# Optimization experiments

Hardware: AMD Instinct MI355X
Metric: run time of the kernel (lower is better)

The kernel has to match this reference:

```python
import jax, jax.numpy as jnp
import numpy as np
from jax import lax

INPUT_DIM = 16
H1, H2 = 64, 32
OUT_DIM = 1
B, T = 4096, 168


def _uniform(key, shape, k):
    return jax.random.uniform(key, shape, jnp.float32, -k, k)


def setup_inputs() -> dict:
    key = jax.random.key(0)
    ks = jax.random.split(key, 12)
    k1 = 1.0 / np.sqrt(H1)
    k2 = 1.0 / np.sqrt(H2)
    return {
        "x": jax.random.normal(ks[0], (B, T, INPUT_DIM), jnp.float32),
        # layer 1 (PyTorch gate order: i, f, g, o)
        "W_ih1": _uniform(ks[1], (4 * H1, INPUT_DIM), k1),
        "W_hh1": _uniform(ks[2], (4 * H1, H1), k1),
        "b_ih1": _uniform(ks[3], (4 * H1,), k1),
        "b_hh1": _uniform(ks[4], (4 * H1,), k1),
        # layer 2
        "W_ih2": _uniform(ks[5], (4 * H2, H1), k2),
        "W_hh2": _uniform(ks[6], (4 * H2, H2), k2),
        "b_ih2": _uniform(ks[7], (4 * H2,), k2),
        "b_hh2": _uniform(ks[8], (4 * H2,), k2),
        # final linear
        "W_fc": _uniform(ks[9], (OUT_DIM, H2), k2),
        "b_fc": _uniform(ks[10], (OUT_DIM,), k2),
    }


def _lstm(x, W_ih, W_hh, b_ih, b_hh, hidden):
    # Precompute input-to-gate projections for all timesteps: [B, T, 4H]
    xg = jnp.einsum("btd,gd->btg", x, W_ih) + b_ih + b_hh

    def step(carry, xt):
        h, c = carry
        gates = xt + h @ W_hh.T  # [B, 4H]
        i, f, g, o = jnp.split(gates, 4, axis=-1)
        i = jax.nn.sigmoid(i)
        f = jax.nn.sigmoid(f)
        g = jnp.tanh(g)
        o = jax.nn.sigmoid(o)
        c = f * c + i * g
        h = o * jnp.tanh(c)
        return (h, c), h

    bsz = x.shape[0]
    init = (jnp.zeros((bsz, hidden), x.dtype), jnp.zeros((bsz, hidden), x.dtype))
    (_, _), hs = lax.scan(step, init, jnp.swapaxes(xg, 0, 1))  # hs: [T, B, H]
    return jnp.swapaxes(hs, 0, 1)  # [B, T, H]


def reference(x, W_ih1, W_hh1, b_ih1, b_hh1, W_ih2, W_hh2, b_ih2, b_hh2, W_fc, b_fc):
    # Dropout layers are identity at inference (p=0.2 in train only).
    h1 = _lstm(x, W_ih1, W_hh1, b_ih1, b_hh1, H1)   # [B, T, 64]
    h2 = _lstm(h1, W_ih2, W_hh2, b_ih2, b_hh2, H2)  # [B, T, 32]
    last = h2[:, -1, :]                              # [B, 32]
    return last @ W_fc.T + b_fc                      # [B, OUT_DIM]
```

## Files before the change

kernel.cpp:

```cpp
#include <hip/hip_runtime.h>


typedef __bf16 bf16x8 __attribute__((ext_vector_type(8)));
typedef float  f32x4  __attribute__((ext_vector_type(4)));

constexpr int T_SEQ = 168;
constexpr int NB    = 16;

__device__ __forceinline__ float fsig(float v)  { return __builtin_amdgcn_rcpf(1.f + __expf(-v)); }
__device__ __forceinline__ float ftanhf(float v){ return 2.f * __builtin_amdgcn_rcpf(1.f + __expf(-2.f * v)) - 1.f; }

__device__ __forceinline__ void split_bf16(float x, __bf16& hi, __bf16& lo) {
  hi = (__bf16)x;
  lo = (__bf16)(x - (float)hi);
}

__device__ __forceinline__ void load_frag8(const float* __restrict__ Wrow, int k0,
                                           bf16x8& hi, bf16x8& lo) {
#pragma unroll
  for (int j = 0; j < 8; ++j) {
    float v = Wrow[k0 + j];
    __bf16 h = (__bf16)v;
    hi[j] = h;
    lo[j] = (__bf16)(v - (float)h);
  }
}

#define MFMA(a, b, c) __builtin_amdgcn_mfma_f32_16x16x32_bf16((a), (b), (c), 0, 0, 0)

__global__ __launch_bounds__(512) __attribute__((amdgpu_waves_per_eu(2, 2)))
void lstm_mfma_kernel(const float* __restrict__ x,
    const float* __restrict__ Wih1, const float* __restrict__ Whh1,
    const float* __restrict__ bih1, const float* __restrict__ bhh1,
    const float* __restrict__ Wih2, const float* __restrict__ Whh2,
    const float* __restrict__ bih2, const float* __restrict__ bhh2,
    const float* __restrict__ Wfc,  const float* __restrict__ bfc,
    float* __restrict__ out)
{
  __shared__ __align__(16) __bf16 sA1[2][4 * 64 * 8];
  __shared__ __align__(16) __bf16 sA2[2][2 * 64 * 8];
  __shared__ __align__(16) __bf16 sW2lo[8 * 2 * 64 * 8];
  __shared__ __align__(16) float  sP[2][2 * 4 * 64 * 4];
  __shared__ __align__(16) float  sH2f[16 * 32];

  const int tid  = threadIdx.x;
  const int w    = tid >> 6;
  const int lane = tid & 63;
  const int q    = lane >> 4;
  const int col  = lane & 15;
  const int b0   = blockIdx.x * NB;

  const bool isL1  = (w < 4);
  const bool isL2b = (w == 4) || (w == 5);
  const bool isL2a = (w >= 6);
  const int  wl2b  = w - 4;
  const int  wl2a  = w - 6;

  bf16x8 bhh[4][4];
  bf16x8 bih[4];
  float  b1v[4] = {0.f, 0.f, 0.f, 0.f};
  if (isL1) {
#pragma unroll
    for (int g = 0; g < 4; ++g) {
      const int r = g * 64 + w * 16 + col;
      const float* Wr = Whh1 + r * 64;
      bf16x8 h0, l0, h1f, l1f;
      load_frag8(Wr, 0 * 32 + q * 8, h0, l0);
      load_frag8(Wr, 1 * 32 + q * 8, h1f, l1f);
      bhh[g][0] = h0; bhh[g][1] = h1f; bhh[g][2] = l0; bhh[g][3] = l1f;
      bf16x8 xh, xl;
      load_frag8(Wih1 + r * 16, (q & 1) * 8, xh, xl);
      bih[g] = (q < 2) ? xh : xl;
      b1v[g] = bih1[r] + bhh1[r];
    }
  }
  bf16x8 wh2h[4], wh2l[4];
  float  b2v[4] = {0.f, 0.f, 0.f, 0.f};
  if (isL2b) {
#pragma unroll
    for (int g = 0; g < 4; ++g) {
      const int r = g * 32 + wl2b * 16 + col;
      bf16x8 hh, ll;
      load_frag8(Whh2 + r * 32, q * 8, hh, ll);
      wh2h[g] = hh; wh2l[g] = ll;
      b2v[g] = bih2[r] + bhh2[r];
    }
  }
  bf16x8 w2ih[4][2];
  if (isL2a) {
#pragma unroll
    for (int g = 0; g < 4; ++g) {
      const int r = g * 32 + wl2a * 16 + col;
#pragma unroll
      for (int kb = 0; kb < 2; ++kb) {
        bf16x8 hh, ll;
        load_frag8(Wih2 + r * 64, kb * 32 + q * 8, hh, ll);
        w2ih[g][kb] = hh;
      }
    }
  }

  for (int idx = tid; idx < 8 * 2 * 64; idx += 512) {
    const int nt  = idx >> 7;
    const int kb2 = (idx >> 6) & 1;
    const int ln  = idx & 63;
    const int qq  = ln >> 4, cc = ln & 15;
    const int g   = nt >> 1, wv = nt & 1;
    const int r   = g * 32 + wv * 16 + cc;
    const int k0  = kb2 * 32 + qq * 8;
    bf16x8 hh, ll;
    load_frag8(Wih2 + r * 64, k0, hh, ll);
    *(bf16x8*)&sW2lo[((nt * 2 + kb2) * 64 + ln) * 8] = ll;
  }

  {
    bf16x8 z;
#pragma unroll
    for (int j = 0; j < 8; ++j) z[j] = (__bf16)0.f;
    for (int i = tid; i < 2 * 4 * 64; i += 512) *(bf16x8*)&sA1[0][i * 8] = z;
    for (int i = tid; i < 2 * 2 * 64; i += 512) *(bf16x8*)&sA2[0][i * 8] = z;
  }
  __syncthreads();

  const float* xbase = x + ((size_t)(b0 + col) * T_SEQ) * 16 + (q & 1) * 8;
  float4 xcA, xcB, xnA, xnB;
  if (isL1) {
    xcA = *(const float4*)(xbase + 0);
    xcB = *(const float4*)(xbase + 4);
  }

  float c1s[4] = {0.f, 0.f, 0.f, 0.f};
  float c2s[4] = {0.f, 0.f, 0.f, 0.f};
  const int uu   = w * 16 + col;
  const int uu2b = wl2b * 16 + col;

  const int kbh  = uu >> 5;
  const int lnb  = ((uu & 31) >> 3) * 16;
  const int jj   = uu & 7;
  const int lnb2 = ((uu2b & 31) >> 3) * 16;
  const int jj2  = uu2b & 7;

#define STEP(Pc, DO_L1, DO_XPRE, DO_L2A, DO_L2B, DO_H2F, TT) do {              \
    if ((DO_L1) && isL1) {                                                     \
      bf16x8 a1[4];                                                            \
      _Pragma("unroll")                                                        \
      for (int kb = 0; kb < 4; ++kb)                                           \
        a1[kb] = *(const bf16x8*)&sA1[(Pc)][(kb * 64 + lane) * 8];             \
      if (DO_XPRE) {                                                           \
        const float* xr = xbase + (size_t)((TT) + 1) * 16;                     \
        xnA = *(const float4*)(xr + 0);                                        \
        xnB = *(const float4*)(xr + 4);                                        \
      }                                                                        \
      const float xc[8] = {xcA.x, xcA.y, xcA.z, xcA.w, xcB.x, xcB.y, xcB.z, xcB.w}; \
      bf16x8 xh8, xl8;                                                         \
      _Pragma("unroll")                                                        \
      for (int j = 0; j < 8; ++j) {                                            \
        __bf16 h_, l_; split_bf16(xc[j], h_, l_);                              \
        xh8[j] = h_; xl8[j] = l_;                                              \
      }                                                                        \
      const bf16x8 ax0 = (q < 2) ? xh8 : xl8;                                  \
      const bf16x8 ax1 = (q < 2) ? xl8 : xh8;                                  \
      f32x4 ca[4], cb[4];                                                      \
      _Pragma("unroll")                                                        \
      for (int g = 0; g < 4; ++g) {                                            \
        ca[g][0] = b1v[g]; ca[g][1] = b1v[g]; ca[g][2] = b1v[g]; ca[g][3] = b1v[g]; \
        cb[g][0] = 0.f; cb[g][1] = 0.f; cb[g][2] = 0.f; cb[g][3] = 0.f;        \
      }                                                                        \
      _Pragma("unroll")                                                        \
      for (int g = 0; g < 4; ++g) {                                            \
        ca[g] = MFMA(ax0,   bih[g],    ca[g]);                                 \
        ca[g] = MFMA(ax1,   bih[g],    ca[g]);                                 \
        ca[g] = MFMA(a1[0], bhh[g][0], ca[g]);                                 \
        ca[g] = MFMA(a1[1], bhh[g][1], ca[g]);                                 \
        cb[g] = MFMA(a1[2], bhh[g][0], cb[g]);                                 \
        cb[g] = MFMA(a1[3], bhh[g][1], cb[g]);                                 \
        cb[g] = MFMA(a1[0], bhh[g][2], cb[g]);                                 \
        cb[g] = MFMA(a1[1], bhh[g][3], cb[g]);                                 \
      }                                                                        \
      _Pragma("unroll")                                                        \
      for (int r = 0; r < 4; ++r) {                                            \
        const float iv = fsig(ca[0][r] + cb[0][r]);                            \
        const float fv = fsig(ca[1][r] + cb[1][r]);                            \
        const float gv = ftanhf(ca[2][r] + cb[2][r]);                          \
        const float ov = fsig(ca[3][r] + cb[3][r]);                            \
        const float cc = fmaf(fv, c1s[r], iv * gv);                            \
        c1s[r] = cc;                                                           \
        __bf16 hh_, hl_;                                                       \
        split_bf16(ov * ftanhf(cc), hh_, hl_);                                 \
        const int m = q * 4 + r;                                               \
        sA1[1 - (Pc)][((kbh * 64) + lnb + m) * 8 + jj]       = hh_;            \
        sA1[1 - (Pc)][(((2 + kbh) * 64) + lnb + m) * 8 + jj] = hl_;            \
      }                                                                        \
      if (DO_XPRE) { xcA = xnA; xcB = xnB; }                                   \
    }                                                                          \
    if ((DO_L2A) && isL2a) {                                                   \
      bf16x8 a2[4];                                                            \
      _Pragma("unroll")                                                        \
      for (int kb = 0; kb < 4; ++kb)                                           \
        a2[kb] = *(const bf16x8*)&sA1[(Pc)][(kb * 64 + lane) * 8];             \
      _Pragma("unroll")                                                        \
      for (int g = 0; g < 4; ++g) {                                            \
        const int nt = g * 2 + wl2a;                                           \
        const bf16x8 bb2 = *(const bf16x8*)&sW2lo[((nt * 2 + 0) * 64 + lane) * 8]; \
        const bf16x8 bb3 = *(const bf16x8*)&sW2lo[((nt * 2 + 1) * 64 + lane) * 8]; \
        f32x4 pa = {0.f, 0.f, 0.f, 0.f};                                       \
        pa = MFMA(a2[0], w2ih[g][0], pa);                         \
        pa = MFMA(a2[1], w2ih[g][1], pa);                                      \
        pa = MFMA(a2[0], bb2, pa);                                \
        pa = MFMA(a2[1], bb3, pa);                                             \
        pa = MFMA(a2[2], w2ih[g][0], pa);                         \
        pa = MFMA(a2[3], w2ih[g][1], pa);                                      \
        *(f32x4*)&sP[(Pc)][((wl2a * 4 + g) * 64 + lane) * 4] = pa;             \
      }                                                                        \
    }                                                                          \
    if ((DO_L2B) && isL2b) {                                                   \
      const bf16x8 ah0 = *(const bf16x8*)&sA2[1 - (Pc)][(0 * 64 + lane) * 8];  \
      const bf16x8 ah1 = *(const bf16x8*)&sA2[1 - (Pc)][(1 * 64 + lane) * 8];  \
      f32x4 c2[4];                                                             \
      _Pragma("unroll")                                                        \
      for (int g = 0; g < 4; ++g) {                                            \
        c2[g][0] = b2v[g]; c2[g][1] = b2v[g]; c2[g][2] = b2v[g]; c2[g][3] = b2v[g]; \
        c2[g] = MFMA(ah0, wh2h[g], c2[g]);                                     \
        c2[g] = MFMA(ah1, wh2h[g], c2[g]);                                     \
        c2[g] = MFMA(ah0, wh2l[g], c2[g]);                                     \
        c2[g] += *(const f32x4*)&sP[1 - (Pc)][((wl2b * 4 + g) * 64 + lane) * 4]; \
      }                                                                        \
      _Pragma("unroll")                                                        \
      for (int r = 0; r < 4; ++r) {                                            \
        const float iv = fsig(c2[0][r]);                                       \
        const float fv = fsig(c2[1][r]);                                       \
        const float gv = ftanhf(c2[2][r]);                                     \
        const float ov = fsig(c2[3][r]);                                       \
        const float cc = fmaf(fv, c2s[r], iv * gv);                            \
        c2s[r] = cc;                                                           \
        const float hf = ov * ftanhf(cc);                                      \
        __bf16 hh_, hl_;                                                       \
        split_bf16(hf, hh_, hl_);                                              \
        const int m = q * 4 + r;                                               \
        sA2[(Pc)][((0 * 64) + lnb2 + m) * 8 + jj2] = hh_;                      \
        sA2[(Pc)][((1 * 64) + lnb2 + m) * 8 + jj2] = hl_;                      \
        if (DO_H2F) sH2f[m * 32 + uu2b] = hf;                                  \
      }                                                                        \
    }                                                                          \
    __syncthreads();                                                           \
  } while (0)

  STEP(0, true,  true,  false, false, false, 0);
  STEP(1, true,  true,  true,  false, false, 1);
  for (int t = 2; t < 166; t += 2) {
    STEP(0, true, true, true, true, false, t);
    STEP(1, true, true, true, true, false, t + 1);
  }
  STEP(0, true,  true,  true,  true,  false, 166);
  STEP(1, true,  false, true,  true,  false, 167);
  STEP(0, false, false, true,  true,  false, 168);
  STEP(1, false, false, false, true,  true,  169);
#undef STEP

  if (tid < NB) {
    float s = bfc[0];
#pragma unroll
    for (int j = 0; j < 32; ++j) s = fmaf(Wfc[j], sH2f[tid * 32 + j], s);
    out[b0 + tid] = s;
  }
}

extern "C" void kernel_launch(void* const* d_in, const int* in_sizes, int n_in,
                              void* d_out, int out_size, void* d_ws, size_t ws_size,
                              hipStream_t stream) {
  (void)in_sizes; (void)n_in; (void)out_size; (void)d_ws; (void)ws_size;
  const float* x    = (const float*)d_in[0];
  const float* Wih1 = (const float*)d_in[1];
  const float* Whh1 = (const float*)d_in[2];
  const float* bih1 = (const float*)d_in[3];
  const float* bhh1 = (const float*)d_in[4];
  const float* Wih2 = (const float*)d_in[5];
  const float* Whh2 = (const float*)d_in[6];
  const float* bih2 = (const float*)d_in[7];
  const float* bhh2 = (const float*)d_in[8];
  const float* Wfc  = (const float*)d_in[9];
  const float* bfc  = (const float*)d_in[10];
  float* out = (float*)d_out;

  hipLaunchKernelGGL(lstm_mfma_kernel, dim3(4096 / NB), dim3(512), 0, stream,
                     x, Wih1, Whh1, bih1, bhh1, Wih2, Whh2, bih2, bhh2, Wfc, bfc, out);
}
```

Measured before the change: 273.5 us.

## Offload layer-1 input projection to layer-2 waves via shared-memory staging

Moves the per-step x·W_ih1 + bias projection off the layer-1 waves, which sit on the critical recurrent path, onto the four layer-2 waves. Those waves compute the projection one step ahead and store it in a double-buffered shared array (sXG). Layer-1 waves then load it as the MFMA accumulator seed, which removes two MFMAs per gate plus the x split work from their step. The cost is extra LDS traffic and more MFMA and global-load work on the layer-2 waves, which could lengthen their part of each step.

Result: slower. 288.1 us (+5.3%).

```diff
diff --git a/kernel.cpp b/kernel.cpp
--- a/kernel.cpp
+++ b/kernel.cpp
@@ -41,6 +41,7 @@
   __shared__ __align__(16) __bf16 sA2[2][2 * 64 * 8];
   __shared__ __align__(16) __bf16 sW2lo[8 * 2 * 64 * 8];
   __shared__ __align__(16) float  sP[2][2 * 4 * 64 * 4];
+  __shared__ __align__(16) float  sXG[2][16 * 64 * 4];
   __shared__ __align__(16) float  sH2f[16 * 32];
 
   const int tid  = threadIdx.x;
@@ -51,14 +52,14 @@
   const int b0   = blockIdx.x * NB;
 
   const bool isL1  = (w < 4);
+  const bool isL2  = (w >= 4);
   const bool isL2b = (w == 4) || (w == 5);
   const bool isL2a = (w >= 6);
   const int  wl2b  = w - 4;
   const int  wl2a  = w - 6;
+  const int  tbase = (w - 4) * 4;
 
   bf16x8 bhh[4][4];
-  bf16x8 bih[4];
-  float  b1v[4] = {0.f, 0.f, 0.f, 0.f};
   if (isL1) {
 #pragma unroll
     for (int g = 0; g < 4; ++g) {
@@ -68,10 +69,6 @@
       load_frag8(Wr, 0 * 32 + q * 8, h0, l0);
       load_frag8(Wr, 1 * 32 + q * 8, h1f, l1f);
       bhh[g][0] = h0; bhh[g][1] = h1f; bhh[g][2] = l0; bhh[g][3] = l1f;
-      bf16x8 xh, xl;
-      load_frag8(Wih1 + r * 16, (q & 1) * 8, xh, xl);
-      bih[g] = (q < 2) ? xh : xl;
-      b1v[g] = bih1[r] + bhh1[r];
     }
   }
   bf16x8 wh2h[4], wh2l[4];
@@ -97,6 +94,18 @@
         load_frag8(Wih2 + r * 64, kb * 32 + q * 8, hh, ll);
         w2ih[g][kb] = hh;
       }
+    }
+  }
+  bf16x8 wxg[4];
+  float  bxg[4] = {0.f, 0.f, 0.f, 0.f};
+  if (isL2) {
+#pragma unroll
+    for (int i = 0; i < 4; ++i) {
+      const int row = (tbase + i) * 16 + col;
+      bf16x8 hh, ll;
+      load_frag8(Wih1 + row * 16, (q & 1) * 8, hh, ll);
+      wxg[i] = (q < 2) ? hh : ll;
+      bxg[i] = bih1[row] + bhh1[row];
     }
   }
 
@@ -120,14 +129,33 @@
     for (int i = tid; i < 2 * 4 * 64; i += 512) *(bf16x8*)&sA1[0][i * 8] = z;
     for (int i = tid; i < 2 * 2 * 64; i += 512) *(bf16x8*)&sA2[0][i * 8] = z;
   }
-  __syncthreads();
 
   const float* xbase = x + ((size_t)(b0 + col) * T_SEQ) * 16 + (q & 1) * 8;
   float4 xcA, xcB, xnA, xnB;
-  if (isL1) {
+  if (isL2) {
     xcA = *(const float4*)(xbase + 0);
     xcB = *(const float4*)(xbase + 4);
-  }
+    const float xcv[8] = {xcA.x, xcA.y, xcA.z, xcA.w, xcB.x, xcB.y, xcB.z, xcB.w};
+    bf16x8 xh8, xl8;
+#pragma unroll
+    for (int j = 0; j < 8; ++j) {
+      __bf16 h_, l_; split_bf16(xcv[j], h_, l_);
+      xh8[j] = h_; xl8[j] = l_;
+    }
+    const bf16x8 ax0 = (q < 2) ? xh8 : xl8;
+    const bf16x8 ax1 = (q < 2) ? xl8 : xh8;
+#pragma unroll
+    for (int i = 0; i < 4; ++i) {
+      f32x4 cx;
+      cx[0] = bxg[i]; cx[1] = bxg[i]; cx[2] = bxg[i]; cx[3] = bxg[i];
+      cx = MFMA(ax0, wxg[i], cx);
+      cx = MFMA(ax1, wxg[i], cx);
+      *(f32x4*)&sXG[0][(((tbase + i) * 64) + lane) * 4] = cx;
+    }
+    xcA = *(const float4*)(xbase + 16);
+    xcB = *(const float4*)(xbase + 20);
+  }
+  __syncthreads();
 
   float c1s[4] = {0.f, 0.f, 0.f, 0.f};
   float c2s[4] = {0.f, 0.f, 0.f, 0.f};
@@ -140,42 +168,27 @@
   const int lnb2 = ((uu2b & 31) >> 3) * 16;
   const int jj2  = uu2b & 7;
 
-#define STEP(Pc, DO_L1, DO_XPRE, DO_L2A, DO_L2B, DO_H2F, TT) do {              \
+  const f32x4 z4 = {0.f, 0.f, 0.f, 0.f};
+
+#define STEP(Pc, DO_L1, DO_XPRE, DO_XG, DO_L2A, DO_L2B, DO_H2F, TT) do {       \
     if ((DO_L1) && isL1) {                                                     \
       bf16x8 a1[4];                                                            \
       _Pragma("unroll")                                                        \
       for (int kb = 0; kb < 4; ++kb)                                           \
         a1[kb] = *(const bf16x8*)&sA1[(Pc)][(kb * 64 + lane) * 8];             \
-      if (DO_XPRE) {                                                           \
-        const float* xr = xbase + (size_t)((TT) + 1) * 16;                     \
-        xnA = *(const float4*)(xr + 0);                                        \
-        xnB = *(const float4*)(xr + 4);                                        \
-      }                                                                        \
-      const float xc[8] = {xcA.x, xcA.y, xcA.z, xcA.w, xcB.x, xcB.y, xcB.z, xcB.w}; \
-      bf16x8 xh8, xl8;                                                         \
-      _Pragma("unroll")                                                        \
-      for (int j = 0; j < 8; ++j) {                                            \
-        __bf16 h_, l_; split_bf16(xc[j], h_, l_);                              \
-        xh8[j] = h_; xl8[j] = l_;                                              \
-      }                                                                        \
-      const bf16x8 ax0 = (q < 2) ? xh8 : xl8;                                  \
-      const bf16x8 ax1 = (q < 2) ? xl8 : xh8;                                  \
+      f32x4 xg[4];                                                             \
+      _Pragma("unroll")                                                        \
+      for (int g = 0; g < 4; ++g)                                              \
+        xg[g] = *(const f32x4*)&sXG[(Pc)][(((g * 4 + w) * 64) + lane) * 4];    \
       f32x4 ca[4], cb[4];                                                      \
       _Pragma("unroll")                                                        \
       for (int g = 0; g < 4; ++g) {                                            \
-        ca[g][0] = b1v[g]; ca[g][1] = b1v[g]; ca[g][2] = b1v[g]; ca[g][3] = b1v[g]; \
-        cb[g][0] = 0.f; cb[g][1] = 0.f; cb[g][2] = 0.f; cb[g][3] = 0.f;        \
-      }                                                                        \
-      _Pragma("unroll")                                                        \
-      for (int g = 0; g < 4; ++g) {                                            \
-        ca[g] = MFMA(ax0,   bih[g],    ca[g]);                                 \
-        ca[g] = MFMA(ax1,   bih[g],    ca[g]);                                 \
-        ca[g] = MFMA(a1[0], bhh[g][0], ca[g]);                                 \
-        ca[g] = MFMA(a1[1], bhh[g][1], ca[g]);                                 \
-        cb[g] = MFMA(a1[2], bhh[g][0], cb[g]);                                 \
-        cb[g] = MFMA(a1[3], bhh[g][1], cb[g]);                                 \
-        cb[g] = MFMA(a1[0], bhh[g][2], cb[g]);                                 \
-        cb[g] = MFMA(a1[1], bhh[g][3], cb[g]);                                 \
+        ca[g] = MFMA(a1[0], bhh[g][0], xg[g]);                \
+        ca[g] = MFMA(a1[1], bhh[g][1], ca[g]);                \
+        ca[g] = MFMA(a1[2], bhh[g][0], ca[g]);                \
+        cb[g] = MFMA(a1[3], bhh[g][1], z4);                   \
+        cb[g] = MFMA(a1[0], bhh[g][2], cb[g]);                \
+        cb[g] = MFMA(a1[1], bhh[g][3], cb[g]);                \
       }                                                                        \
       _Pragma("unroll")                                                        \
       for (int r = 0; r < 4; ++r) {                                            \
@@ -191,7 +204,6 @@
         sA1[1 - (Pc)][((kbh * 64) + lnb + m) * 8 + jj]       = hh_;            \
         sA1[1 - (Pc)][(((2 + kbh) * 64) + lnb + m) * 8 + jj] = hl_;            \
       }                                                                        \
-      if (DO_XPRE) { xcA = xnA; xcB = xnB; }                                   \
     }                                                                          \
     if ((DO_L2A) && isL2a) {                                                   \
       bf16x8 a2[4];                                                            \
@@ -242,19 +254,44 @@
         if (DO_H2F) sH2f[m * 32 + uu2b] = hf;                                  \
       }                                                                        \
     }                                                                          \
+    if ((DO_XG) && isL2) {                \
+      if (DO_XPRE) {                                                           \
+        const float* xr = xbase + (size_t)((TT) + 2) * 16;                     \
+        xnA = *(const float4*)(xr + 0);                                        \
+        xnB = *(const float4*)(xr + 4);                                        \
+      }                                                                        \
+      const float xcv[8] = {xcA.x, xcA.y, xcA.z, xcA.w, xcB.x, xcB.y, xcB.z, xcB.w}; \
+      bf16x8 xh8, xl8;                                                         \
+      _Pragma("unroll")                                                        \
+      for (int j = 0; j < 8; ++j) {                                            \
+        __bf16 h_, l_; split_bf16(xcv[j], h_, l_);                             \
+        xh8[j] = h_; xl8[j] = l_;                                              \
+      }                                                                        \
+      const bf16x8 ax0 = (q < 2) ? xh8 : xl8;                                  \
+      const bf16x8 ax1 = (q < 2) ? xl8 : xh8;                                  \
+      _Pragma("unroll")                                                        \
+      for (int i = 0; i < 4; ++i) {                                            \
+        f32x4 cx;                                                              \
+        cx[0] = bxg[i]; cx[1] = bxg[i]; cx[2] = bxg[i]; cx[3] = bxg[i];        \
+        cx = MFMA(ax0, wxg[i], cx);                                            \
+        cx = MFMA(ax1, wxg[i], cx);                                            \
+        *(f32x4*)&sXG[1 - (Pc)][(((tbase + i) * 64) + lane) * 4] = cx;         \
+      }                                                                        \
+      if (DO_XPRE) { xcA = xnA; xcB = xnB; }                                   \
+    }                                                                          \
     __syncthreads();                                                           \
   } while (0)
 
-  STEP(0, true,  true,  false, false, false, 0);
-  STEP(1, true,  true,  true,  false, false, 1);
+  STEP(0, true,  true,  true,  false, false, false, 0);
+  STEP(1, true,  true,  true,  true,  false, false, 1);
   for (int t = 2; t < 166; t += 2) {
-    STEP(0, true, true, true, true, false, t);
-    STEP(1, true, true, true, true, false, t + 1);
-  }
-  STEP(0, true,  true,  true,  true,  false, 166);
-  STEP(1, true,  false, true,  true,  false, 167);
-  STEP(0, false, false, true,  true,  false, 168);
-  STEP(1, false, false, false, true,  true,  169);
+    STEP(0, true, true, true, true, true, false, t);
+    STEP(1, true, true, true, true, true, false, t + 1);
+  }
+  STEP(0, true,  false, true,  true,  true,  false, 166);
+  STEP(1, true,  false, false, true,  true,  false, 167);
+  STEP(0, false, false, false, true,  true,  false, 168);
+  STEP(1, false, false, false, false, true,  true,  169);
 #undef STEP
 
   if (tid < NB) {
```
